# Kernel tuning notes

Measured on AMD Instinct MI355X. Metric: run time of the kernel, lower is better.

## Reference

```python
import jax, jax.numpy as jnp
import numpy as np

B, S, H, L, C = 32, 512, 768, 512, 3  # batch, seq, hidden, max_length, num_classes


def _lin_init(k, fan_in, shape):
    return jax.random.normal(k, shape, jnp.float32) * (1.0 / np.sqrt(fan_in))


def setup_inputs() -> dict:
    key = jax.random.key(0)
    ks = jax.random.split(key, 18)
    return {
        "tokens": jax.random.normal(ks[0], (B, S, H), jnp.float32),
        # shared Q/K/V projections (used for both token- and feature-attention)
        "Wq": _lin_init(ks[1], H, (H, H)), "bq": jnp.zeros((H,), jnp.float32),
        "Wk": _lin_init(ks[2], H, (H, H)), "bk": jnp.zeros((H,), jnp.float32),
        "Wv": _lin_init(ks[3], H, (H, H)), "bv": jnp.zeros((H,), jnp.float32),
        # TSGSA: Linear(H,1)+ReLU gate over tokens
        "W_ts": _lin_init(ks[4], H, (H, 1)), "b_ts": jnp.zeros((1,), jnp.float32),
        # FSGSA: Linear(max_length,1)+ReLU gate over padded seq axis (also reused for FGSA per source bug)
        "W_fs": _lin_init(ks[5], L, (L, 1)), "b_fs": jnp.zeros((1,), jnp.float32),
        # TGSA: Linear(H,H)+Sigmoid gate
        "W_tg": _lin_init(ks[6], H, (H, H)), "b_tg": jnp.zeros((H,), jnp.float32),
        # fnn: Linear(7H,H) -> Linear(H,C)
        "W1": _lin_init(ks[7], 7 * H, (7 * H, H)), "b1": jnp.zeros((H,), jnp.float32),
        "W2": _lin_init(ks[8], H, (H, C)), "b2": jnp.zeros((C,), jnp.float32),
    }


def _ln(x):
    # LayerNorm over (seq, hidden) jointly, eps=1e-8; freshly-instantiated affine params are identity
    m = jnp.mean(x, axis=(1, 2), keepdims=True)
    v = jnp.var(x, axis=(1, 2), keepdims=True)
    return (x - m) * jax.lax.rsqrt(v + 1e-8)


def reference(tokens, Wq, bq, Wk, bk, Wv, bv, W_ts, b_ts, W_fs, b_fs, W_tg, b_tg, W1, b1, W2, b2):
    scale = 1.0 / np.sqrt(H)
    Q = tokens @ Wq + bq  # [B,S,H]
    K = tokens @ Wk + bk
    V = tokens @ Wv + bv
    # token-direction self-attention: softmax(Q K^T / sqrt(H)) V
    att = jax.nn.softmax(jnp.einsum('bsh,bth->bst', Q, K) * scale, axis=-1)  # [B,S,S]
    TSA = jnp.einsum('bst,bth->bsh', att, V)
    # feature-direction self-attention: V @ softmax(Q^T K / sqrt(H))
    attN = jax.nn.softmax(jnp.einsum('bsh,bsg->bhg', Q, K) * scale, axis=-1)  # [B,H,H]
    FSA = jnp.einsum('bsh,bhg->bsg', V, attN)
    # gate branches
    TSGSA = jax.nn.relu(tokens @ W_ts + b_ts) * tokens  # [B,S,1]*[B,S,H]
    tpad = jnp.pad(tokens.transpose(0, 2, 1), ((0, 0), (0, 0), (0, L - S)))  # [B,H,L]
    gate_f = jax.nn.relu(tpad @ W_fs + b_fs)  # [B,H,1]
    FSGSA = (gate_f * tokens.transpose(0, 2, 1)).transpose(0, 2, 1)  # [B,S,H]
    TGSA = jax.nn.sigmoid(tokens @ W_tg + b_tg) * tokens
    FGSA = FSGSA  # source bug: FGSA branch applies self.FSGSA, identical to FSGSA
    out_all = jnp.concatenate(
        [tokens, _ln(TSA), _ln(FSA), _ln(TGSA), _ln(FGSA), _ln(TSGSA), _ln(FSGSA)], axis=2)  # [B,S,7H]
    pooled = jnp.mean(out_all, axis=1)  # [B,7H]
    return (pooled @ W1 + b1) @ W2 + b2  # [B,C]
```

## Files before the change

kernel.cpp:

```cpp
#include <hip/hip_runtime.h>
#include <cmath>

typedef unsigned short u16;
typedef __attribute__((ext_vector_type(4))) float f32x4;
typedef __attribute__((ext_vector_type(4))) unsigned int u32x4;
typedef __attribute__((ext_vector_type(8))) __bf16 bf16x8;

__device__ __forceinline__ u16 f2b(float f) {
  unsigned int u = __builtin_bit_cast(unsigned int, f);
  return (u16)((u + 0x7fffu + ((u >> 16) & 1u)) >> 16);
}
__device__ __forceinline__ float b2f(u16 h) {
  unsigned int u = ((unsigned int)h) << 16;
  return __builtin_bit_cast(float, u);
}

__device__ __forceinline__ void glds16(const u16* g, u16* l) {
  __builtin_amdgcn_global_load_lds(
      (const __attribute__((address_space(1))) void*)g,
      (__attribute__((address_space(3))) void*)l, 16, 0, 0);
}

template <int EPI>
__global__ __launch_bounds__(512) void gemm_f_k(
    const u16* __restrict__ Ap, const u16* __restrict__ Bp, u16* __restrict__ Cp,
    u16* __restrict__ CpT, const float* __restrict__ bias,
    const u16* __restrict__ tokp, float* __restrict__ colsum,
    float* __restrict__ bstat, int K, int lda, int ldb, int ldc, long sA,
    long sB, long sC, float scale) {
  __shared__ alignas(16) u16 Asm[2][8192];
  __shared__ alignas(16) u16 Bsm[2][4096];
  __shared__ float scol_s[128];
  __shared__ float sred[2];

  const int gx = gridDim.x, gxy = gx * gridDim.y;
  const int nwg = gxy * gridDim.z;
  int orig = (blockIdx.z * gridDim.y + blockIdx.y) * gx + blockIdx.x;
  int gwi = (orig & 7) * (nwg >> 3) + (orig >> 3);
  const int z = gwi / gxy;
  int rem = gwi - z * gxy;
  const int ty = rem / gx, tx = rem - ty * gx;
  const int tileM = ty << 8, tileN = tx << 7;

  const u16* Abase = Ap + (size_t)z * sA;
  const u16* Bbase = Bp + (size_t)z * sB;

  const int tid = threadIdx.x;
  const int lane = tid & 63, w = tid >> 6;
  const int wr = (w >> 1) << 6, wc = (w & 1) << 6;
  const int fr = lane & 15, fg = lane >> 4;

  f32x4 acc[4][4];
#pragma unroll
  for (int i = 0; i < 4; ++i)
#pragma unroll
    for (int j = 0; j < 4; ++j) acc[i][j] = (f32x4){0.f, 0.f, 0.f, 0.f};

  const int sArow = (w << 5) + (lane >> 2);
  const int sBrow = (w << 4) + (lane >> 2);
  const int scol = (((lane & 3) ^ ((lane >> 3) & 3)) << 3);
  const u16* gA = Abase + (size_t)(tileM + sArow) * lda + scol;
  const u16* gB = Bbase + (size_t)(tileN + sBrow) * ldb + scol;
  const int ldsA = (w << 5) * 32;
  const int ldsB = (w << 4) * 32;

  auto STAGE = [&](int buf, int k0) {
    glds16(gA + k0, &Asm[buf][ldsA]);
    glds16(gA + (size_t)16 * lda + k0, &Asm[buf][ldsA + 512]);
    glds16(gB + k0, &Bsm[buf][ldsB]);
  };

  const int col_off = ((fg ^ ((fr >> 1) & 3)) << 3);

  const int nt = K >> 5;
  STAGE(0, 0);
  int cur = 0;
  for (int t = 0; t < nt; ++t) {
    if (t + 1 < nt) {
      STAGE(cur ^ 1, (t + 1) << 5);
      asm volatile("s_waitcnt vmcnt(3)" ::: "memory");
    } else {
      asm volatile("s_waitcnt vmcnt(0)" ::: "memory");
    }
    __builtin_amdgcn_s_barrier();
    asm volatile("" ::: "memory");
    const u16* Ab = Asm[cur];
    const u16* Bb = Bsm[cur];
    bf16x8 av[4], bw[4];
#pragma unroll
    for (int m = 0; m < 4; ++m)
      av[m] = *(const bf16x8*)&Ab[(wr + (m << 4) + fr) * 32 + col_off];
#pragma unroll
    for (int n = 0; n < 4; ++n)
      bw[n] = *(const bf16x8*)&Bb[(wc + (n << 4) + fr) * 32 + col_off];
#pragma unroll
    for (int m = 0; m < 4; ++m)
#pragma unroll
      for (int n = 0; n < 4; ++n)
        acc[m][n] =
            __builtin_amdgcn_mfma_f32_16x16x32_bf16(av[m], bw[n], acc[m][n], 0, 0, 0);
    asm volatile("" ::: "memory");
    __builtin_amdgcn_s_barrier();
    cur ^= 1;
  }

  if constexpr (EPI == 0) {
    const int cbuf = tileN / 768;
    const int nbase = tileN - cbuf * 768;
    u16* Cz = Cp + (size_t)cbuf * sC;
#pragma unroll
    for (int m = 0; m < 4; ++m) {
#pragma unroll
      for (int n = 0; n < 4; ++n) {
        const int gcol = tileN + wc + (n << 4) + fr;
        const int lcol = nbase + wc + (n << 4) + fr;
        const float bv2 = bias[gcol];
#pragma unroll
        for (int r = 0; r < 4; ++r) {
          const int grow = tileM + wr + (m << 4) + (fg << 2) + r;
          Cz[(size_t)grow * 768 + lcol] = f2b(acc[m][n][r] + bv2);
        }
      }
    }
    u16* Ct = CpT + (size_t)cbuf * sC;
    const int zb = tileM >> 9;
    const int sbase = tileM & 511;
#pragma unroll
    for (int m = 0; m < 4; ++m) {
#pragma unroll
      for (int n = 0; n < 4; ++n) {
        const int gcol = tileN + wc + (n << 4) + fr;
        const int lcol = nbase + wc + (n << 4) + fr;
        const int srow0 = sbase + wr + (m << 4) + (fg << 2);
        union { u16 u[4]; unsigned long long q; } pk;
#pragma unroll
        for (int r = 0; r < 4; ++r) pk.u[r] = f2b(acc[m][n][r] + bias[gcol]);
        *(unsigned long long*)&Ct[((size_t)(zb * 768 + lcol) << 9) + srow0] = pk.q;
      }
    }
  } else if constexpr (EPI == 1) {
    if (tid < 128) scol_s[tid] = 0.f;
    if (tid == 0) { sred[0] = 0.f; sred[1] = 0.f; }
    __syncthreads();
    float ls = 0.f, lq = 0.f;
#pragma unroll
    for (int n = 0; n < 4; ++n) {
      float cpart = 0.f;
      const int gcol = tileN + wc + (n << 4) + fr;
      const float bv2 = bias[gcol];
#pragma unroll
      for (int m = 0; m < 4; ++m) {
#pragma unroll
        for (int r = 0; r < 4; ++r) {
          const int grow = tileM + wr + (m << 4) + (fg << 2) + r;
          float g = 1.f / (1.f + __expf(-(acc[m][n][r] + bv2)));
          float v = g * b2f(tokp[(size_t)grow * 768 + gcol]);
          cpart += v; ls += v; lq += v * v;
        }
      }
      atomicAdd(&scol_s[wc + (n << 4) + fr], cpart);
    }
    atomicAdd(&sred[0], ls);
    atomicAdd(&sred[1], lq);
    __syncthreads();
    const int b = tileM >> 9;
    if (tid < 128) atomicAdd(&colsum[(size_t)b * 768 + tileN + tid], scol_s[tid]);
    if (tid == 0) {
      atomicAdd(&bstat[b], sred[0]);
      atomicAdd(&bstat[32 + b], sred[1]);
    }
  } else if constexpr (EPI == 2) {
    u16* Cz = Cp + (size_t)z * sC;
#pragma unroll
    for (int m = 0; m < 4; ++m) {
#pragma unroll
      for (int n = 0; n < 4; ++n) {
        const int gcol = tileN + wc + (n << 4) + fr;
#pragma unroll
        for (int r = 0; r < 4; ++r) {
          const int grow = tileM + wr + (m << 4) + (fg << 2) + r;
          Cz[(size_t)grow * ldc + gcol] = f2b(acc[m][n][r] * scale);
        }
      }
    }
  } else if constexpr (EPI == 4) {
    u16* Cz = Cp + (size_t)z * sC;
    float lmax[4];
#pragma unroll
    for (int n = 0; n < 4; ++n) {
      const int gcol = tileN + wc + (n << 4) + fr;
      float mx = -1e30f;
#pragma unroll
      for (int m = 0; m < 4; ++m) {
#pragma unroll
        for (int r = 0; r < 4; ++r) {
          const int grow = tileM + wr + (m << 4) + (fg << 2) + r;
          float v = acc[m][n][r] * scale;
          Cz[(size_t)grow * ldc + gcol] = f2b(v);
          mx = fmaxf(mx, v);
        }
      }
      lmax[n] = mx;
    }
    float* red = (float*)&Asm[0][0];
    const int slot = ((w >> 1) << 2) + fg;
    __syncthreads();
#pragma unroll
    for (int n = 0; n < 4; ++n)
      red[slot * 132 + wc + (n << 4) + fr] = lmax[n];
    __syncthreads();
    if (tid < 128) {
      float m2 = red[tid];
#pragma unroll
      for (int i = 1; i < 16; ++i) m2 = fmaxf(m2, red[i * 132 + tid]);
      scol_s[tid] = m2;
    }
    __syncthreads();
    float lsum[4];
#pragma unroll
    for (int n = 0; n < 4; ++n) {
      const float M = scol_s[wc + (n << 4) + fr];
      float s2 = 0.f;
#pragma unroll
      for (int m = 0; m < 4; ++m)
#pragma unroll
        for (int r = 0; r < 4; ++r) s2 += __expf(acc[m][n][r] * scale - M);
      lsum[n] = s2;
    }
    __syncthreads();
#pragma unroll
    for (int n = 0; n < 4; ++n)
      red[slot * 132 + wc + (n << 4) + fr] = lsum[n];
    __syncthreads();
    if (tid < 128) {
      float s2 = 0.f;
#pragma unroll
      for (int i = 0; i < 16; ++i) s2 += red[i * 132 + tid];
      const int ty3 = tileM >> 8;
      const size_t pidx = ((size_t)z * 3 + ty3) * 768 + tileN + tid;
      colsum[pidx] = scol_s[tid];
      bstat[pidx] = s2;
    }
  } else {
    if (tid < 128) scol_s[tid] = 0.f;
    if (tid == 0) { sred[0] = 0.f; sred[1] = 0.f; }
    __syncthreads();
    float ls = 0.f, lq = 0.f;
#pragma unroll
    for (int n = 0; n < 4; ++n) {
      float cpart = 0.f;
#pragma unroll
      for (int m = 0; m < 4; ++m) {
#pragma unroll
        for (int r = 0; r < 4; ++r) {
          float v = acc[m][n][r];
          cpart += v; ls += v; lq += v * v;
        }
      }
      atomicAdd(&scol_s[wc + (n << 4) + fr], cpart);
    }
    atomicAdd(&sred[0], ls);
    atomicAdd(&sred[1], lq);
    __syncthreads();
    if (tid < 128) atomicAdd(&colsum[(size_t)z * 768 + tileN + tid], scol_s[tid]);
    if (tid == 0) {
      atomicAdd(&bstat[z], sred[0]);
      atomicAdd(&bstat[32 + z], sred[1]);
    }
  }
}

__global__ __launch_bounds__(256) void cvt_row_k(
    const float* __restrict__ tok, u16* __restrict__ tokb,
    const float* __restrict__ Wts, const float* __restrict__ bts,
    float* __restrict__ gate_t, float* __restrict__ rowsum,
    float* __restrict__ rowsumsq) {
  const int w = threadIdx.x >> 6, lane = threadIdx.x & 63;
  const int row = blockIdx.x * 4 + w;
  const float* p = tok + (size_t)row * 768;
  u16* q = tokb + (size_t)row * 768;
  float s = 0.f, sq = 0.f, g = 0.f;
#pragma unroll
  for (int i = 0; i < 3; ++i) {
    const int idx = (i * 64 + lane) << 2;
    f32x4 v = *(const f32x4*)(p + idx);
    f32x4 wv = *(const f32x4*)(Wts + idx);
    union { u16 u[4]; unsigned long long q8; } pk;
#pragma unroll
    for (int j = 0; j < 4; ++j) {
      s += v[j]; sq += v[j] * v[j]; g += v[j] * wv[j];
      pk.u[j] = f2b(v[j]);
    }
    *(unsigned long long*)(q + idx) = pk.q8;
  }
#pragma unroll
  for (int o = 32; o > 0; o >>= 1) {
    s += __shfl_xor(s, o); sq += __shfl_xor(sq, o); g += __shfl_xor(g, o);
  }
  if (lane == 0) {
    gate_t[row] = fmaxf(g + bts[0], 0.f);
    rowsum[row] = s;
    rowsumsq[row] = sq;
  }
}

__global__ __launch_bounds__(256) void transpose_w_k(const float* __restrict__ W,
                                                     u16* __restrict__ WT) {
  __shared__ float t[64][65];
  const int r0 = blockIdx.y << 6, c0 = blockIdx.x << 6;
  for (int i = threadIdx.x; i < 4096; i += 256) {
    int r = i >> 6, c = i & 63;
    t[r][c] = W[(size_t)(r0 + r) * 768 + c0 + c];
  }
  __syncthreads();
  for (int i = threadIdx.x; i < 4096; i += 256) {
    int rr = i >> 6, cc = i & 63;
    WT[(size_t)(c0 + rr) * 768 + r0 + cc] = f2b(t[cc][rr]);
  }
}

template <int LEN>
__global__ __launch_bounds__(256) void softmax_k(u16* __restrict__ data) {
  constexpr int NP = LEN / 256;
  const int row = blockIdx.x, tid = threadIdx.x;
  u16* p = data + (size_t)row * LEN;
  const int lane = tid & 63, wid = tid >> 6;
  float v[NP];
  float mx = -1e30f;
#pragma unroll
  for (int i = 0; i < NP; ++i) { v[i] = b2f(p[tid + (i << 8)]); mx = fmaxf(mx, v[i]); }
#pragma unroll
  for (int o = 32; o > 0; o >>= 1) mx = fmaxf(mx, __shfl_xor(mx, o));
  __shared__ float red[4], red2[4];
  if (lane == 0) red[wid] = mx;
  __syncthreads();
  mx = fmaxf(fmaxf(red[0], red[1]), fmaxf(red[2], red[3]));
  float sum = 0.f;
#pragma unroll
  for (int i = 0; i < NP; ++i) { v[i] = __expf(v[i] - mx); sum += v[i]; }
#pragma unroll
  for (int o = 32; o > 0; o >>= 1) sum += __shfl_xor(sum, o);
  if (lane == 0) red2[wid] = sum;
  __syncthreads();
  sum = red2[0] + red2[1] + red2[2] + red2[3];
  const float inv = 1.f / sum;
#pragma unroll
  for (int i = 0; i < NP; ++i) p[tid + (i << 8)] = f2b(v[i] * inv);
}

__global__ __launch_bounds__(256) void colnorm_k(u16* __restrict__ data,
                                                 const float* __restrict__ pmax,
                                                 const float* __restrict__ psum) {
  __shared__ u16 tile[32][72];
  const int tid = threadIdx.x;
  const int b = blockIdx.x;
  u16* base = data + (size_t)b * 589824 + (blockIdx.y << 6);
  const int lr = tid >> 3, seg = (tid & 7) << 3;
  const int c = tid & 63, q = tid >> 6;
  const size_t p0 = (size_t)b * 3 * 768 + (blockIdx.y << 6) + c;
  const float m0 = pmax[p0], m1 = pmax[p0 + 768], m2 = pmax[p0 + 1536];
  const float M = fmaxf(fmaxf(m0, m1), m2);
  const float S = psum[p0] * __expf(m0 - M) + psum[p0 + 768] * __expf(m1 - M) +
                  psum[p0 + 1536] * __expf(m2 - M);
  const float inv = 1.f / S;
  for (int ch = 0; ch < 24; ++ch) {
    u16* g = base + (size_t)(ch * 32 + lr) * 768 + seg;
    *(u32x4*)&tile[lr][seg] = *(const u32x4*)g;
    __syncthreads();
#pragma unroll
    for (int i = 0; i < 8; ++i) {
      const int r = (q << 3) + i;
      tile[r][c] = f2b(__expf(b2f(tile[r][c]) - M) * inv);
    }
    __syncthreads();
    *(u32x4*)g = *(const u32x4*)&tile[lr][seg];
    __syncthreads();
  }
}

__global__ __launch_bounds__(256) void col_stats_k(
    const u16* __restrict__ tokb, const float* __restrict__ Wfs,
    const float* __restrict__ bfs, const float* __restrict__ gate_t,
    float* __restrict__ gate_f, float* __restrict__ colsum_tok,
    float* __restrict__ colsumsq_tok, float* __restrict__ colsum_tsg) {
  const int b = blockIdx.x, h = blockIdx.y * 256 + threadIdx.x;
  const u16* p = tokb + (size_t)b * 512 * 768 + h;
  const float* gt = gate_t + b * 512;
  float cs = 0.f, cq = 0.f, gf = 0.f, tg = 0.f;
#pragma unroll 4
  for (int s = 0; s < 512; ++s) {
    float t = b2f(p[(size_t)s * 768]);
    cs += t; cq += t * t; gf += t * Wfs[s]; tg += t * gt[s];
  }
  const int idx = b * 768 + h;
  gate_f[idx] = fmaxf(gf + bfs[0], 0.f);
  colsum_tok[idx] = cs;
  colsumsq_tok[idx] = cq;
  colsum_tsg[idx] = tg;
}

__global__ __launch_bounds__(256) void batch_stats_k(
    const float* __restrict__ gate_t, const float* __restrict__ rowsum,
    const float* __restrict__ rowsumsq, const float* __restrict__ gate_f,
    const float* __restrict__ colsum_tok, const float* __restrict__ colsumsq_tok,
    float* __restrict__ st) {
  __shared__ float red[4][256];
  const int b = blockIdx.x, tid = threadIdx.x;
  float ts = 0.f, tq = 0.f, fs = 0.f, fq = 0.f;
  for (int s = tid; s < 512; s += 256) {
    float g = gate_t[b * 512 + s];
    ts += g * rowsum[b * 512 + s];
    tq += g * g * rowsumsq[b * 512 + s];
  }
  for (int h = tid; h < 768; h += 256) {
    float g = gate_f[b * 768 + h];
    fs += g * colsum_tok[b * 768 + h];
    fq += g * g * colsumsq_tok[b * 768 + h];
  }
  red[0][tid] = ts; red[1][tid] = tq; red[2][tid] = fs; red[3][tid] = fq;
  __syncthreads();
  for (int o = 128; o > 0; o >>= 1) {
    if (tid < o) {
      red[0][tid] += red[0][tid + o];
      red[1][tid] += red[1][tid + o];
      red[2][tid] += red[2][tid + o];
      red[3][tid] += red[3][tid + o];
    }
    __syncthreads();
  }
  if (tid == 0) {
    st[b] = red[0][0]; st[32 + b] = red[1][0];
    st[64 + b] = red[2][0]; st[96 + b] = red[3][0];
  }
}

__global__ __launch_bounds__(768) void pooled_k(
    const float* __restrict__ colsum_tok, const float* __restrict__ colsum_tsa,
    const float* __restrict__ bstat_tsa, const float* __restrict__ colsum_fsa,
    const float* __restrict__ bstat_fsa, const float* __restrict__ colsum_tgsa,
    const float* __restrict__ bstat_tgsa, const float* __restrict__ colsum_tsg,
    const float* __restrict__ gate_f, const float* __restrict__ st,
    float* __restrict__ pooled) {
  const int b = blockIdx.x, h = threadIdx.x;
  const float invS = 1.f / 512.f, invN = 1.f / (512.f * 768.f);
  const int i = b * 768 + h;
  float* pr = pooled + (size_t)b * 5376;
  pr[h] = colsum_tok[i] * invS;
  auto lnslot = [&](int slot, float cs, float bs, float bq) {
    float m = bs * invN;
    float var = bq * invN - m * m;
    pr[slot * 768 + h] = (cs * invS - m) * rsqrtf(var + 1e-8f);
  };
  lnslot(1, colsum_tsa[i], bstat_tsa[b], bstat_tsa[32 + b]);
  lnslot(2, colsum_fsa[i], bstat_fsa[b], bstat_fsa[32 + b]);
  lnslot(3, colsum_tgsa[i], bstat_tgsa[b], bstat_tgsa[32 + b]);
  const float fsg_cs = gate_f[i] * colsum_tok[i];
  lnslot(4, fsg_cs, st[64 + b], st[96 + b]);
  lnslot(5, colsum_tsg[i], st[b], st[32 + b]);
  lnslot(6, fsg_cs, st[64 + b], st[96 + b]);
}

__global__ __launch_bounds__(256) void fnn1_k(const float* __restrict__ pooled,
                                              const float* __restrict__ W1,
                                              float* __restrict__ tmp1) {
  __shared__ float sp[128][36];
  const int c0 = blockIdx.x << 7, k0 = blockIdx.y << 7;
  const int tid = threadIdx.x;
  for (int i = tid; i < 4096; i += 256) {
    int b = i >> 7, j = i & 127;
    sp[j][b] = pooled[(size_t)b * 5376 + k0 + j];
  }
  __syncthreads();
  const int c = c0 + (tid & 127);
  const int u = (tid >> 7) << 4;
  float acc[16];
#pragma unroll
  for (int t = 0; t < 16; ++t) acc[t] = 0.f;
#pragma unroll 4
  for (int j = 0; j < 128; ++j) {
    float w = W1[(size_t)(k0 + j) * 768 + c];
    const f32x4* row = (const f32x4*)&sp[j][u];
#pragma unroll
    for (int t4 = 0; t4 < 4; ++t4) {
      f32x4 v = row[t4];
#pragma unroll
      for (int r = 0; r < 4; ++r) acc[t4 * 4 + r] += v[r] * w;
    }
  }
#pragma unroll
  for (int t = 0; t < 16; ++t) atomicAdd(&tmp1[(u + t) * 768 + c], acc[t]);
}

__global__ __launch_bounds__(256) void fnn2_k(const float* __restrict__ tmp1,
                                              const float* __restrict__ b1,
                                              const float* __restrict__ W2,
                                              const float* __restrict__ b2,
                                              float* __restrict__ out) {
  const int gw = blockIdx.x * 4 + (threadIdx.x >> 6);
  const int lane = threadIdx.x & 63;
  const int b = gw / 3, c = gw % 3;
  float a = 0.f;
#pragma unroll
  for (int i = 0; i < 12; ++i) {
    int k = lane + i * 64;
    a += (tmp1[b * 768 + k] + b1[k]) * W2[k * 3 + c];
  }
#pragma unroll
  for (int o = 32; o > 0; o >>= 1) a += __shfl_xor(a, o);
  if (lane == 0) out[b * 3 + c] = a + b2[c];
}

extern "C" void kernel_launch(void* const* d_in, const int* in_sizes, int n_in,
                              void* d_out, int out_size, void* d_ws, size_t ws_size,
                              hipStream_t stream) {
  const float* tokens = (const float*)d_in[0];
  const float* Wq = (const float*)d_in[1];
  const float* bq = (const float*)d_in[2];
  const float* Wk = (const float*)d_in[3];
  const float* bk = (const float*)d_in[4];
  const float* Wv = (const float*)d_in[5];
  const float* bv = (const float*)d_in[6];
  const float* Wts = (const float*)d_in[7];
  const float* bts = (const float*)d_in[8];
  const float* Wfs = (const float*)d_in[9];
  const float* bfs = (const float*)d_in[10];
  const float* Wtg = (const float*)d_in[11];
  const float* btg = (const float*)d_in[12];
  const float* W1 = (const float*)d_in[13];
  const float* b1 = (const float*)d_in[14];
  const float* W2 = (const float*)d_in[15];
  const float* b2 = (const float*)d_in[16];
  float* out = (float*)d_out;

  char* ws = (char*)d_ws;
  size_t off = 0;
  auto take = [&](size_t bytes) -> char* {
    char* p = ws + off;
    off += (bytes + 255) & ~(size_t)255;
    return p;
  };
  u16* tokb = (u16*)take((size_t)16384 * 768 * 2);
  u16* WqT = (u16*)take((size_t)768 * 768 * 2);
  u16* WkT = (u16*)take((size_t)768 * 768 * 2);
  u16* WvT = (u16*)take((size_t)768 * 768 * 2);
  u16* WtgT = (u16*)take((size_t)768 * 768 * 2);
  u16* Qb = (u16*)take((size_t)16384 * 768 * 2);
  u16* Kb = (u16*)take((size_t)16384 * 768 * 2);
  u16* Vb = (u16*)take((size_t)16384 * 768 * 2);
  u16* Qt = (u16*)take((size_t)32 * 768 * 512 * 2);
  u16* Kt = (u16*)take((size_t)32 * 768 * 512 * 2);
  u16* Vt = (u16*)take((size_t)32 * 768 * 512 * 2);
  u16* attb = (u16*)take((size_t)32 * 512 * 512 * 2);
  u16* attNt = (u16*)take((size_t)32 * 768 * 768 * 2);
  float* bias3 = (float*)take(2304 * 4);
  float* pmax = (float*)take((size_t)32 * 3 * 768 * 4);
  float* psum = (float*)take((size_t)32 * 3 * 768 * 4);
  char* zbase = ws + off;
  float* colsum_tsa = (float*)take(24576 * 4);
  float* colsum_fsa = (float*)take(24576 * 4);
  float* colsum_tgsa = (float*)take(24576 * 4);
  float* bstat_tsa = (float*)take(64 * 4);
  float* bstat_fsa = (float*)take(64 * 4);
  float* bstat_tgsa = (float*)take(64 * 4);
  float* tmp1 = (float*)take((size_t)32 * 768 * 4);
  size_t zbytes = (size_t)((ws + off) - zbase);
  float* colsum_tsg = (float*)take(24576 * 4);
  float* gate_t = (float*)take(16384 * 4);
  float* rowsum = (float*)take(16384 * 4);
  float* rowsumsq = (float*)take(16384 * 4);
  float* gate_f = (float*)take(24576 * 4);
  float* colsum_tok = (float*)take(24576 * 4);
  float* colsumsq_tok = (float*)take(24576 * 4);
  float* st4 = (float*)take(128 * 4);
  float* pooled = (float*)take((size_t)32 * 5376 * 4);

  hipMemsetAsync(zbase, 0, zbytes, stream);
  hipMemcpyAsync(bias3, bq, 768 * 4, hipMemcpyDeviceToDevice, stream);
  hipMemcpyAsync(bias3 + 768, bk, 768 * 4, hipMemcpyDeviceToDevice, stream);
  hipMemcpyAsync(bias3 + 1536, bv, 768 * 4, hipMemcpyDeviceToDevice, stream);

  const float scale = 1.0f / sqrtf(768.0f);
  const dim3 blk(256);
  const dim3 blk512(512);

  cvt_row_k<<<4096, blk, 0, stream>>>(tokens, tokb, Wts, bts, gate_t, rowsum,
                                      rowsumsq);
  transpose_w_k<<<dim3(12, 12), blk, 0, stream>>>(Wq, WqT);
  transpose_w_k<<<dim3(12, 12), blk, 0, stream>>>(Wk, WkT);
  transpose_w_k<<<dim3(12, 12), blk, 0, stream>>>(Wv, WvT);
  transpose_w_k<<<dim3(12, 12), blk, 0, stream>>>(Wtg, WtgT);

  gemm_f_k<0><<<dim3(18, 64, 1), blk512, 0, stream>>>(
      tokb, WqT, Qb, Qt, bias3, nullptr, nullptr, nullptr, 768, 768, 768, 768,
      0, 0, 12582912, 0.f);
  gemm_f_k<1><<<dim3(6, 64, 1), blk512, 0, stream>>>(
      tokb, WtgT, nullptr, nullptr, btg, tokb, colsum_tgsa, bstat_tgsa, 768,
      768, 768, 0, 0, 0, 0, 0.f);

  gemm_f_k<4><<<dim3(6, 3, 32), blk512, 0, stream>>>(
      Kt, Qt, attNt, nullptr, nullptr, nullptr, pmax, psum, 512, 512, 512, 768,
      393216, 393216, 589824, scale);
  colnorm_k<<<dim3(32, 12), blk, 0, stream>>>(attNt, pmax, psum);

  gemm_f_k<2><<<dim3(4, 2, 32), blk512, 0, stream>>>(
      Qb, Kb, attb, nullptr, nullptr, nullptr, nullptr, nullptr, 768, 768, 768,
      512, 393216, 393216, 262144, scale);
  softmax_k<512><<<16384, 256, 0, stream>>>(attb);

  gemm_f_k<3><<<dim3(6, 2, 32), blk512, 0, stream>>>(
      attb, Vt, nullptr, nullptr, nullptr, nullptr, colsum_tsa, bstat_tsa, 512,
      512, 512, 0, 262144, 393216, 0, 0.f);
  gemm_f_k<3><<<dim3(6, 2, 32), blk512, 0, stream>>>(
      Vb, attNt, nullptr, nullptr, nullptr, nullptr, colsum_fsa, bstat_fsa, 768,
      768, 768, 0, 393216, 589824, 0, 0.f);

  col_stats_k<<<dim3(32, 3), blk, 0, stream>>>(tokb, Wfs, bfs, gate_t, gate_f,
                                               colsum_tok, colsumsq_tok, colsum_tsg);
  batch_stats_k<<<32, blk, 0, stream>>>(gate_t, rowsum, rowsumsq, gate_f,
                                        colsum_tok, colsumsq_tok, st4);

  pooled_k<<<32, 768, 0, stream>>>(colsum_tok, colsum_tsa, bstat_tsa, colsum_fsa,
                                   bstat_fsa, colsum_tgsa, bstat_tgsa, colsum_tsg,
                                   gate_f, st4, pooled);
  fnn1_k<<<dim3(6, 42), blk, 0, stream>>>(pooled, W1, tmp1);
  fnn2_k<<<24, blk, 0, stream>>>(tmp1, b1, W2, b2, out);
}
```

Baseline: 418.8 us.

## Fold softmax normalization into GEMM epilogues and drop separate softmax passes

Both softmaxes are restructured. The score GEMMs now write unnormalized exp values with no max subtraction and accumulate row or column sums. The token-attention normalization is applied per row inside the attention-V GEMM epilogue. The feature-attention normalization is folded into a pre-scaled copy of V, which reuses the Qt buffer. This removes the standalone softmax and column-normalize kernels and their read-modify-write passes over large bf16 buffers, and the four weight transposes are merged into one launch. Skipping max subtraction risks overflow or precision loss if scores grow large, and it relies on Qt being dead by then.

```diff
diff --git a/kernel.cpp b/kernel.cpp
--- a/kernel.cpp
+++ b/kernel.cpp
@@ -26,11 +26,12 @@
     const u16* __restrict__ Ap, const u16* __restrict__ Bp, u16* __restrict__ Cp,
     u16* __restrict__ CpT, const float* __restrict__ bias,
     const u16* __restrict__ tokp, float* __restrict__ colsum,
-    float* __restrict__ bstat, int K, int lda, int ldb, int ldc, long sA,
-    long sB, long sC, float scale) {
+    float* __restrict__ bstat, const float* __restrict__ rs, int K, int lda,
+    int ldb, int ldc, long sA, long sB, long sC, float scale) {
   __shared__ alignas(16) u16 Asm[2][8192];
   __shared__ alignas(16) u16 Bsm[2][4096];
   __shared__ float scol_s[128];
+  __shared__ float scrow[256];
   __shared__ float sred[2];
 
   const int gx = gridDim.x, gxy = gx * gridDim.y;
@@ -169,77 +170,106 @@
       atomicAdd(&bstat[b], sred[0]);
       atomicAdd(&bstat[32 + b], sred[1]);
     }
-  } else if constexpr (EPI == 2) {
+  } else if constexpr (EPI == 4) {
     u16* Cz = Cp + (size_t)z * sC;
-#pragma unroll
-    for (int m = 0; m < 4; ++m) {
-#pragma unroll
-      for (int n = 0; n < 4; ++n) {
-        const int gcol = tileN + wc + (n << 4) + fr;
+    float lsum[4];
+#pragma unroll
+    for (int n = 0; n < 4; ++n) {
+      const int gcol = tileN + wc + (n << 4) + fr;
+      float s2 = 0.f;
+#pragma unroll
+      for (int m = 0; m < 4; ++m) {
 #pragma unroll
         for (int r = 0; r < 4; ++r) {
           const int grow = tileM + wr + (m << 4) + (fg << 2) + r;
-          Cz[(size_t)grow * ldc + gcol] = f2b(acc[m][n][r] * scale);
+          float e = __expf(acc[m][n][r] * scale);
+          Cz[(size_t)grow * ldc + gcol] = f2b(e);
+          s2 += e;
         }
       }
-    }
-  } else if constexpr (EPI == 4) {
+      lsum[n] = s2;
+    }
+    float* red = (float*)&Asm[0][0];
+    const int slot = ((w >> 1) << 2) + fg;
+    __syncthreads();
+#pragma unroll
+    for (int n = 0; n < 4; ++n)
+      red[slot * 132 + wc + (n << 4) + fr] = lsum[n];
+    __syncthreads();
+    if (tid < 128) {
+      float s2 = 0.f;
+#pragma unroll
+      for (int i = 0; i < 16; ++i) s2 += red[i * 132 + tid];
+      const int ty3 = tileM >> 8;
+      colsum[((size_t)z * 3 + ty3) * 768 + tileN + tid] = s2;
+    }
+  } else if constexpr (EPI == 5) {
     u16* Cz = Cp + (size_t)z * sC;
-    float lmax[4];
+    if (tid < 256) scrow[tid] = 0.f;
+    __syncthreads();
+    float rpart[4][4];
+#pragma unroll
+    for (int m = 0; m < 4; ++m)
+#pragma unroll
+      for (int r = 0; r < 4; ++r) rpart[m][r] = 0.f;
 #pragma unroll
     for (int n = 0; n < 4; ++n) {
       const int gcol = tileN + wc + (n << 4) + fr;
-      float mx = -1e30f;
 #pragma unroll
       for (int m = 0; m < 4; ++m) {
 #pragma unroll
         for (int r = 0; r < 4; ++r) {
           const int grow = tileM + wr + (m << 4) + (fg << 2) + r;
-          float v = acc[m][n][r] * scale;
-          Cz[(size_t)grow * ldc + gcol] = f2b(v);
-          mx = fmaxf(mx, v);
+          float e = __expf(acc[m][n][r] * scale);
+          Cz[(size_t)grow * ldc + gcol] = f2b(e);
+          rpart[m][r] += e;
         }
       }
-      lmax[n] = mx;
-    }
-    float* red = (float*)&Asm[0][0];
-    const int slot = ((w >> 1) << 2) + fg;
-    __syncthreads();
-#pragma unroll
-    for (int n = 0; n < 4; ++n)
-      red[slot * 132 + wc + (n << 4) + fr] = lmax[n];
-    __syncthreads();
-    if (tid < 128) {
-      float m2 = red[tid];
-#pragma unroll
-      for (int i = 1; i < 16; ++i) m2 = fmaxf(m2, red[i * 132 + tid]);
-      scol_s[tid] = m2;
-    }
-    __syncthreads();
-    float lsum[4];
+    }
+#pragma unroll
+    for (int m = 0; m < 4; ++m) {
+#pragma unroll
+      for (int r = 0; r < 4; ++r) {
+        float v = rpart[m][r];
+        v += __shfl_xor(v, 1); v += __shfl_xor(v, 2);
+        v += __shfl_xor(v, 4); v += __shfl_xor(v, 8);
+        if (fr == 0) atomicAdd(&scrow[wr + (m << 4) + (fg << 2) + r], v);
+      }
+    }
+    __syncthreads();
+    if (tid < 256) atomicAdd(&colsum[(size_t)z * 512 + tileM + tid], scrow[tid]);
+  } else if constexpr (EPI == 6) {
+    float isr[4][4];
+#pragma unroll
+    for (int m = 0; m < 4; ++m)
+#pragma unroll
+      for (int r = 0; r < 4; ++r)
+        isr[m][r] =
+            1.f / rs[(size_t)z * 512 + tileM + wr + (m << 4) + (fg << 2) + r];
+    if (tid < 128) scol_s[tid] = 0.f;
+    if (tid == 0) { sred[0] = 0.f; sred[1] = 0.f; }
+    __syncthreads();
+    float ls = 0.f, lq = 0.f;
 #pragma unroll
     for (int n = 0; n < 4; ++n) {
-      const float M = scol_s[wc + (n << 4) + fr];
-      float s2 = 0.f;
-#pragma unroll
-      for (int m = 0; m < 4; ++m)
-#pragma unroll
-        for (int r = 0; r < 4; ++r) s2 += __expf(acc[m][n][r] * scale - M);
-      lsum[n] = s2;
-    }
-    __syncthreads();
-#pragma unroll
-    for (int n = 0; n < 4; ++n)
-      red[slot * 132 + wc + (n << 4) + fr] = lsum[n];
-    __syncthreads();
-    if (tid < 128) {
-      float s2 = 0.f;
-#pragma unroll
-      for (int i = 0; i < 16; ++i) s2 += red[i * 132 + tid];
-      const int ty3 = tileM >> 8;
-      const size_t pidx = ((size_t)z * 3 + ty3) * 768 + tileN + tid;
-      colsum[pidx] = scol_s[tid];
-      bstat[pidx] = s2;
+      float cpart = 0.f;
+#pragma unroll
+      for (int m = 0; m < 4; ++m) {
+#pragma unroll
+        for (int r = 0; r < 4; ++r) {
+          float v = acc[m][n][r] * isr[m][r];
+          cpart += v; ls += v; lq += v * v;
+        }
+      }
+      atomicAdd(&scol_s[wc + (n << 4) + fr], cpart);
+    }
+    atomicAdd(&sred[0], ls);
+    atomicAdd(&sred[1], lq);
+    __syncthreads();
+    if (tid < 128) atomicAdd(&colsum[(size_t)z * 768 + tileN + tid], scol_s[tid]);
+    if (tid == 0) {
+      atomicAdd(&bstat[z], sred[0]);
+      atomicAdd(&bstat[32 + z], sred[1]);
     }
   } else {
     if (tid < 128) scol_s[tid] = 0.f;
@@ -304,8 +334,13 @@
   }
 }
 
-__global__ __launch_bounds__(256) void transpose_w_k(const float* __restrict__ W,
-                                                     u16* __restrict__ WT) {
+__global__ __launch_bounds__(256) void transpose_w4_k(
+    const float* __restrict__ W0, const float* __restrict__ W1,
+    const float* __restrict__ W2, const float* __restrict__ W3,
+    u16* __restrict__ WT) {
+  const float* W = blockIdx.z == 0 ? W0 : blockIdx.z == 1 ? W1
+                   : blockIdx.z == 2 ? W2 : W3;
+  u16* dst = WT + (size_t)blockIdx.z * 589824;
   __shared__ float t[64][65];
   const int r0 = blockIdx.y << 6, c0 = blockIdx.x << 6;
   for (int i = threadIdx.x; i < 4096; i += 256) {
@@ -315,66 +350,29 @@
   __syncthreads();
   for (int i = threadIdx.x; i < 4096; i += 256) {
     int rr = i >> 6, cc = i & 63;
-    WT[(size_t)(c0 + rr) * 768 + r0 + cc] = f2b(t[cc][rr]);
-  }
-}
-
-template <int LEN>
-__global__ __launch_bounds__(256) void softmax_k(u16* __restrict__ data) {
-  constexpr int NP = LEN / 256;
-  const int row = blockIdx.x, tid = threadIdx.x;
-  u16* p = data + (size_t)row * LEN;
-  const int lane = tid & 63, wid = tid >> 6;
-  float v[NP];
-  float mx = -1e30f;
-#pragma unroll
-  for (int i = 0; i < NP; ++i) { v[i] = b2f(p[tid + (i << 8)]); mx = fmaxf(mx, v[i]); }
-#pragma unroll
-  for (int o = 32; o > 0; o >>= 1) mx = fmaxf(mx, __shfl_xor(mx, o));
-  __shared__ float red[4], red2[4];
-  if (lane == 0) red[wid] = mx;
+    dst[(size_t)(c0 + rr) * 768 + r0 + cc] = f2b(t[cc][rr]);
+  }
+}
+
+__global__ __launch_bounds__(256) void v2scale_k(const u16* __restrict__ Vb,
+                                                 const float* __restrict__ psum,
+                                                 u16* __restrict__ V2) {
+  __shared__ float inv[768];
+  const int z = blockIdx.x, sb = blockIdx.y;
+  const float* pz = psum + (size_t)z * 2304;
+  for (int h = threadIdx.x; h < 768; h += 256)
+    inv[h] = 1.f / (pz[h] + pz[h + 768] + pz[h + 1536]);
   __syncthreads();
-  mx = fmaxf(fmaxf(red[0], red[1]), fmaxf(red[2], red[3]));
-  float sum = 0.f;
-#pragma unroll
-  for (int i = 0; i < NP; ++i) { v[i] = __expf(v[i] - mx); sum += v[i]; }
-#pragma unroll
-  for (int o = 32; o > 0; o >>= 1) sum += __shfl_xor(sum, o);
-  if (lane == 0) red2[wid] = sum;
-  __syncthreads();
-  sum = red2[0] + red2[1] + red2[2] + red2[3];
-  const float inv = 1.f / sum;
-#pragma unroll
-  for (int i = 0; i < NP; ++i) p[tid + (i << 8)] = f2b(v[i] * inv);
-}
-
-__global__ __launch_bounds__(256) void colnorm_k(u16* __restrict__ data,
-                                                 const float* __restrict__ pmax,
-                                                 const float* __restrict__ psum) {
-  __shared__ u16 tile[32][72];
-  const int tid = threadIdx.x;
-  const int b = blockIdx.x;
-  u16* base = data + (size_t)b * 589824 + (blockIdx.y << 6);
-  const int lr = tid >> 3, seg = (tid & 7) << 3;
-  const int c = tid & 63, q = tid >> 6;
-  const size_t p0 = (size_t)b * 3 * 768 + (blockIdx.y << 6) + c;
-  const float m0 = pmax[p0], m1 = pmax[p0 + 768], m2 = pmax[p0 + 1536];
-  const float M = fmaxf(fmaxf(m0, m1), m2);
-  const float S = psum[p0] * __expf(m0 - M) + psum[p0 + 768] * __expf(m1 - M) +
-                  psum[p0 + 1536] * __expf(m2 - M);
-  const float inv = 1.f / S;
-  for (int ch = 0; ch < 24; ++ch) {
-    u16* g = base + (size_t)(ch * 32 + lr) * 768 + seg;
-    *(u32x4*)&tile[lr][seg] = *(const u32x4*)g;
-    __syncthreads();
-#pragma unroll
-    for (int i = 0; i < 8; ++i) {
-      const int r = (q << 3) + i;
-      tile[r][c] = f2b(__expf(b2f(tile[r][c]) - M) * inv);
-    }
-    __syncthreads();
-    *(u32x4*)g = *(const u32x4*)&tile[lr][seg];
-    __syncthreads();
+  const size_t base = (size_t)z * 393216 + (size_t)sb * 64 * 768;
+  for (int i = 0; i < 24; ++i) {
+    const int u = i * 256 + threadIdx.x;
+    const int row = u / 96, seg = (u - row * 96) * 8;
+    const size_t idx = base + (size_t)row * 768 + seg;
+    union { u32x4 q; u16 us[8]; } in, ot;
+    in.q = *(const u32x4*)&Vb[idx];
+#pragma unroll
+    for (int j = 0; j < 8; ++j) ot.us[j] = f2b(b2f(in.us[j]) * inv[seg + j]);
+    *(u32x4*)&V2[idx] = ot.q;
   }
 }
 
@@ -553,8 +551,8 @@
   u16* attb = (u16*)take((size_t)32 * 512 * 512 * 2);
   u16* attNt = (u16*)take((size_t)32 * 768 * 768 * 2);
   float* bias3 = (float*)take(2304 * 4);
-  float* pmax = (float*)take((size_t)32 * 3 * 768 * 4);
   float* psum = (float*)take((size_t)32 * 3 * 768 * 4);
+  u16* V2 = Qt;
   char* zbase = ws + off;
   float* colsum_tsa = (float*)take(24576 * 4);
   float* colsum_fsa = (float*)take(24576 * 4);
@@ -562,6 +560,7 @@
   float* bstat_tsa = (float*)take(64 * 4);
   float* bstat_fsa = (float*)take(64 * 4);
   float* bstat_tgsa = (float*)take(64 * 4);
+  float* rowsumE = (float*)take((size_t)32 * 512 * 4);
   float* tmp1 = (float*)take((size_t)32 * 768 * 4);
   size_t zbytes = (size_t)((ws + off) - zbase);
   float* colsum_tsg = (float*)take(24576 * 4);
@@ -585,34 +584,30 @@
 
   cvt_row_k<<<4096, blk, 0, stream>>>(tokens, tokb, Wts, bts, gate_t, rowsum,
                                       rowsumsq);
-  transpose_w_k<<<dim3(12, 12), blk, 0, stream>>>(Wq, WqT);
-  transpose_w_k<<<dim3(12, 12), blk, 0, stream>>>(Wk, WkT);
-  transpose_w_k<<<dim3(12, 12), blk, 0, stream>>>(Wv, WvT);
-  transpose_w_k<<<dim3(12, 12), blk, 0, stream>>>(Wtg, WtgT);
+  transpose_w4_k<<<dim3(12, 12, 4), blk, 0, stream>>>(Wq, Wk, Wv, Wtg, WqT);
 
   gemm_f_k<0><<<dim3(18, 64, 1), blk512, 0, stream>>>(
-      tokb, WqT, Qb, Qt, bias3, nullptr, nullptr, nullptr, 768, 768, 768, 768,
-      0, 0, 12582912, 0.f);
+      tokb, WqT, Qb, Qt, bias3, nullptr, nullptr, nullptr, nullptr, 768, 768,
+      768, 768, 0, 0, 12582912, 0.f);
   gemm_f_k<1><<<dim3(6, 64, 1), blk512, 0, stream>>>(
-      tokb, WtgT, nullptr, nullptr, btg, tokb, colsum_tgsa, bstat_tgsa, 768,
-      768, 768, 0, 0, 0, 0, 0.f);
+      tokb, WtgT, nullptr, nullptr, btg, tokb, colsum_tgsa, bstat_tgsa, nullptr,
+      768, 768, 768, 0, 0, 0, 0, 0.f);
 
   gemm_f_k<4><<<dim3(6, 3, 32), blk512, 0, stream>>>(
-      Kt, Qt, attNt, nullptr, nullptr, nullptr, pmax, psum, 512, 512, 512, 768,
-      393216, 393216, 589824, scale);
-  colnorm_k<<<dim3(32, 12), blk, 0, stream>>>(attNt, pmax, psum);
-
-  gemm_f_k<2><<<dim3(4, 2, 32), blk512, 0, stream>>>(
-      Qb, Kb, attb, nullptr, nullptr, nullptr, nullptr, nullptr, 768, 768, 768,
-      512, 393216, 393216, 262144, scale);
-  softmax_k<512><<<16384, 256, 0, stream>>>(attb);
-
+      Kt, Qt, attNt, nullptr, nullptr, nullptr, psum, nullptr, nullptr, 512,
+      512, 512, 768, 393216, 393216, 589824, scale);
+  v2scale_k<<<dim3(32, 8), blk, 0, stream>>>(Vb, psum, V2);
+
+  gemm_f_k<5><<<dim3(4, 2, 32), blk512, 0, stream>>>(
+      Qb, Kb, attb, nullptr, nullptr, nullptr, rowsumE, nullptr, nullptr, 768,
+      768, 768, 512, 393216, 393216, 262144, scale);
+
+  gemm_f_k<6><<<dim3(6, 2, 32), blk512, 0, stream>>>(
+      attb, Vt, nullptr, nullptr, nullptr, nullptr, colsum_tsa, bstat_tsa,
+      rowsumE, 512, 512, 512, 0, 262144, 393216, 0, 0.f);
   gemm_f_k<3><<<dim3(6, 2, 32), blk512, 0, stream>>>(
-      attb, Vt, nullptr, nullptr, nullptr, nullptr, colsum_tsa, bstat_tsa, 512,
-      512, 512, 0, 262144, 393216, 0, 0.f);
-  gemm_f_k<3><<<dim3(6, 2, 32), blk512, 0, stream>>>(
-      Vb, attNt, nullptr, nullptr, nullptr, nullptr, colsum_fsa, bstat_fsa, 768,
-      768, 768, 0, 393216, 589824, 0, 0.f);
+      V2, attNt, nullptr, nullptr, nullptr, nullptr, colsum_fsa, bstat_fsa,
+      nullptr, 768, 768, 768, 0, 393216, 589824, 0, 0.f);
 
   col_stats_k<<<dim3(32, 3), blk, 0, stream>>>(tokb, Wfs, bfs, gate_t, gate_f,
                                                colsum_tok, colsumsq_tok, colsum_tsg);
```

Measured after the change: 386.3 us (median of 2 runs). 7.8% less time.
